# Performance work log

Hardware: AMD Instinct MI355X
Metric: run time of the kernel (lower is better)

Reference implementation:

```python
import jax, jax.numpy as jnp
import numpy as np

NUM_HEADS = 16
EMBED_DIM = 1024
HEAD_DIM = EMBED_DIM // NUM_HEADS
SCALE = HEAD_DIM * -0.5  # faithful to source: multiplicative, negative


def setup_inputs() -> dict:
    key = jax.random.key(0)
    kx, kq, kk, kv, ko = jax.random.split(key, 5)
    B, S, E = 2, 2048, EMBED_DIM
    std = 1.0 / np.sqrt(E)
    return {
        "x": jax.random.normal(kx, (B, S, E), dtype=jnp.float32),
        "Wq": jax.random.normal(kq, (E, E), dtype=jnp.float32) * std,
        "Wk": jax.random.normal(kk, (E, E), dtype=jnp.float32) * std,
        "Wv": jax.random.normal(kv, (E, E), dtype=jnp.float32) * std,
        "Wo": jax.random.normal(ko, (E, E), dtype=jnp.float32) * std,
    }


def reference(x, Wq, Wk, Wv, Wo):
    B, S, E = x.shape
    H, D = NUM_HEADS, HEAD_DIM
    # nn.Linear(bias=False): y = x @ W.T
    q = (x @ Wq.T).reshape(B, S, H, D).transpose(0, 2, 1, 3)  # unused downstream (faithful to source)
    k = (x @ Wk.T).reshape(B, S, H, D).transpose(0, 2, 1, 3)  # [B,H,S,D]
    v = (x @ Wv.T).reshape(B, S, H, D).transpose(0, 2, 1, 3)
    # Source bug reproduced: logits = K @ V^T, scaled by head_dim * -0.5
    logits = jnp.einsum('bhsd,bhtd->bhst', k, v) * SCALE  # [B,H,S,S]
    attn = jax.nn.softmax(logits, axis=-1)
    out = jnp.einsum('bhst,bhtd->bhsd', attn, v)  # [B,H,S,D]
    out = out.transpose(0, 2, 1, 3).reshape(B, S, E)
    return out @ Wo.T
```

## Files before the change

### kernel.cpp

```cpp
#include <hip/hip_runtime.h>
#include <math.h>

#define B_ 2
#define S_ 2048
#define E_ 1024
#define H_ 16
#define D_ 64
#define M_ (B_ * S_)
#define SC2 (-46.166241308446828f)

typedef unsigned short u16;
typedef __attribute__((ext_vector_type(8))) short short8;
typedef __attribute__((ext_vector_type(16))) float f32x16;

static __device__ __forceinline__ u16 bf16_rne(float x) {
    unsigned u = __float_as_uint(x);
    u += 0x7FFFu + ((u >> 16) & 1u);
    return (u16)(u >> 16);
}
static __device__ __forceinline__ float bf16f(u16 h) {
    return __uint_as_float(((unsigned)h) << 16);
}
static __device__ __forceinline__ f32x16 mfma_b(short8 a, short8 b, f32x16 c) {
    return __builtin_amdgcn_mfma_f32_32x32x16_bf16(a, b, c, 0, 0, 0);
}
static __device__ __forceinline__ unsigned pack2(u16 a, u16 b) {
    return (unsigned)a | ((unsigned)b << 16);
}
static __device__ __forceinline__ unsigned pack_trunc(float a, float b) {
    return __builtin_amdgcn_perm(__float_as_uint(b), __float_as_uint(a), 0x07060302u);
}
#define ROWMAP(r, hh) (((r) & 3) + ((((r) >> 2)) << 3) + ((hh) << 2))

__global__ __launch_bounds__(256)
void convert_split(const float* __restrict__ x, const float* __restrict__ Wk,
                   const float* __restrict__ Wv, const float* __restrict__ Wo,
                   u16* __restrict__ Xh, u16* __restrict__ Xl,
                   u16* __restrict__ Wkh, u16* __restrict__ Wkl,
                   u16* __restrict__ Wvh, u16* __restrict__ Wvl,
                   u16* __restrict__ Woh, u16* __restrict__ Wol)
{
    const int blk = blockIdx.x;
    const float* src; u16 *dh, *dl; int base; float sc = 1.0f;
    if (blk < 4096)      { src = x;  dh = Xh;  dl = Xl;  base = blk; }
    else if (blk < 5120) { src = Wk; dh = Wkh; dl = Wkl; base = blk - 4096; sc = SC2; }
    else if (blk < 6144) { src = Wv; dh = Wvh; dl = Wvl; base = blk - 5120; }
    else                 { src = Wo; dh = Woh; dl = Wol; base = blk - 6144; }
    const size_t off = ((size_t)base * 256 + threadIdx.x) * 4;
    const float4 v = *(const float4*)(src + off);
    const float f[4] = {v.x * sc, v.y * sc, v.z * sc, v.w * sc};
    u16 h4[4], l4[4];
#pragma unroll
    for (int i = 0; i < 4; ++i) {
        h4[i] = bf16_rne(f[i]);
        l4[i] = bf16_rne(f[i] - bf16f(h4[i]));
    }
    *(uint2*)(dh + off) = make_uint2(pack2(h4[0], h4[1]), pack2(h4[2], h4[3]));
    *(uint2*)(dl + off) = make_uint2(pack2(l4[0], l4[1]), pack2(l4[2], l4[3]));
}

#define CSB 1032
#define ARR (4 * CSB)

template<int MODE>
__global__ __launch_bounds__(512, 2)
void gemm_k(const u16* __restrict__ Ah, const u16* __restrict__ Al,
            const u16* __restrict__ B1h, const u16* __restrict__ B1l,
            const u16* __restrict__ B2h, const u16* __restrict__ B2l,
            u16* __restrict__ Khg, u16* __restrict__ Klg,
            u16* __restrict__ Vhg, u16* __restrict__ Vlg,
            u16* __restrict__ Vtg, float* __restrict__ Cout)
{
    __shared__ u16 stage[(MODE == 0 ? 6 : 4) * ARR];

    const int tid = threadIdx.x;
    const int w = tid >> 6, l31 = tid & 31, hh = (tid >> 5) & 1;
    const int wt = w & 3, ws = w >> 2;
    const int wm = (wt >> 1) << 6, wn = (wt & 1) << 6;
    const int m0 = blockIdx.y * 128, n0 = blockIdx.x * 128;
    const int ch = (ws << 1) + hh;

    const int srow = tid >> 2;
    const int sch  = tid & 3;
    const size_t gA = (size_t)(m0 + srow) * E_ + (sch << 3);
    const size_t gB = (size_t)(n0 + srow) * E_ + (sch << 3);
    const int slo = sch * CSB + srow * 8;

    f32x16 acc1[2][2], acc2[2][2];
#pragma unroll
    for (int mt = 0; mt < 2; ++mt)
#pragma unroll
        for (int nt = 0; nt < 2; ++nt)
#pragma unroll
            for (int r = 0; r < 16; ++r) {
                acc1[mt][nt][r] = 0.f;
                if constexpr (MODE == 0) acc2[mt][nt][r] = 0.f;
            }

    short8 pf[6];
    auto load_tile = [&](int k0) {
        pf[0] = *(const short8*)(Ah + gA + k0);
        pf[2] = *(const short8*)(B1h + gB + k0);
        if constexpr (MODE == 0) {
            pf[1] = *(const short8*)(Al + gA + k0);
            pf[3] = *(const short8*)(B1l + gB + k0);
            pf[4] = *(const short8*)(B2h + gB + k0);
            pf[5] = *(const short8*)(B2l + gB + k0);
        }
    };
    auto store_tile = [&]() {
        *(short8*)&stage[0 * ARR + slo] = pf[0];
        *(short8*)&stage[2 * ARR + slo] = pf[2];
        if constexpr (MODE == 0) {
            *(short8*)&stage[1 * ARR + slo] = pf[1];
            *(short8*)&stage[3 * ARR + slo] = pf[3];
            *(short8*)&stage[4 * ARR + slo] = pf[4];
            *(short8*)&stage[5 * ARR + slo] = pf[5];
        }
    };

    load_tile(0);
    for (int it = 0; it < 32; ++it) {
        store_tile();
        __syncthreads();
        if (it + 1 < 32) load_tile((it + 1) << 5);

        const int aoff = ch * CSB;
        short8 a_h[2], a_l[2];
        a_h[0] = *(const short8*)&stage[0 * ARR + aoff + (wm + l31) * 8];
        a_h[1] = *(const short8*)&stage[0 * ARR + aoff + (wm + 32 + l31) * 8];
        if constexpr (MODE == 0) {
            a_l[0] = *(const short8*)&stage[1 * ARR + aoff + (wm + l31) * 8];
            a_l[1] = *(const short8*)&stage[1 * ARR + aoff + (wm + 32 + l31) * 8];
        }
#pragma unroll
        for (int nt = 0; nt < 2; ++nt) {
            const int ro = aoff + (wn + (nt << 5) + l31) * 8;
            const short8 b1h = *(const short8*)&stage[2 * ARR + ro];
            if constexpr (MODE == 0) {
                const short8 b1l = *(const short8*)&stage[3 * ARR + ro];
                const short8 b2h = *(const short8*)&stage[4 * ARR + ro];
                const short8 b2l = *(const short8*)&stage[5 * ARR + ro];
#pragma unroll
                for (int mt = 0; mt < 2; ++mt) {
                    acc1[mt][nt] = mfma_b(a_h[mt], b1h, acc1[mt][nt]);
                    acc1[mt][nt] = mfma_b(a_h[mt], b1l, acc1[mt][nt]);
                    acc1[mt][nt] = mfma_b(a_l[mt], b1h, acc1[mt][nt]);
                    acc2[mt][nt] = mfma_b(a_h[mt], b2h, acc2[mt][nt]);
                    acc2[mt][nt] = mfma_b(a_h[mt], b2l, acc2[mt][nt]);
                    acc2[mt][nt] = mfma_b(a_l[mt], b2h, acc2[mt][nt]);
                }
            } else {
#pragma unroll
                for (int mt = 0; mt < 2; ++mt)
                    acc1[mt][nt] = mfma_b(a_h[mt], b1h, acc1[mt][nt]);
            }
        }
        __syncthreads();
    }

    float* red = (float*)stage;
    auto merge = [&](f32x16 (&acc)[2][2]) {
#pragma unroll
        for (int mt = 0; mt < 2; ++mt) {
            __syncthreads();
            if (ws == 1) {
#pragma unroll
                for (int nt = 0; nt < 2; ++nt)
#pragma unroll
                    for (int r = 0; r < 16; ++r)
                        red[wt * 2048 + ROWMAP(r, hh) * 64 + (nt << 5) + l31] = acc[mt][nt][r];
            }
            __syncthreads();
            if (ws == 0) {
#pragma unroll
                for (int nt = 0; nt < 2; ++nt)
#pragma unroll
                    for (int r = 0; r < 16; ++r)
                        acc[mt][nt][r] += red[wt * 2048 + ROWMAP(r, hh) * 64 + (nt << 5) + l31];
            }
        }
    };
    merge(acc1);
    if constexpr (MODE == 0) merge(acc2);

    if (ws != 0) return;

#pragma unroll
    for (int nt = 0; nt < 2; ++nt) {
        const int n = n0 + wn + (nt << 5) + l31;
        if constexpr (MODE == 1) {
#pragma unroll
            for (int mt = 0; mt < 2; ++mt)
#pragma unroll
                for (int r = 0; r < 16; ++r) {
                    const int m = m0 + wm + (mt << 5) + ROWMAP(r, hh);
                    Cout[(size_t)m * E_ + n] = acc1[mt][nt][r];
                }
        } else {
            const int hd = n >> 6, d = n & 63;
            const int b = m0 >> 11;
#pragma unroll
            for (int mt = 0; mt < 2; ++mt) {
                u16 vhi[16];
#pragma unroll
                for (int r = 0; r < 16; ++r) {
                    const int s = (m0 + wm + (mt << 5) + ROWMAP(r, hh)) & (S_ - 1);
                    const size_t ib = (((size_t)(b * H_ + hd) << 11) + s) * D_ + d;
                    const float kv = acc1[mt][nt][r];
                    const u16 kh_ = bf16_rne(kv);
                    Khg[ib] = kh_;
                    Klg[ib] = bf16_rne(kv - bf16f(kh_));
                    const float vv = acc2[mt][nt][r];
                    const u16 vh_ = bf16_rne(vv);
                    vhi[r] = vh_;
                    Vhg[ib] = vh_;
                    Vlg[ib] = bf16_rne(vv - bf16f(vh_));
                }
                const size_t vtb = ((size_t)(b * H_ + hd) * D_ + d) << 11;
#pragma unroll
                for (int g = 0; g < 4; ++g) {
                    const int s0 = ((m0 + wm + (mt << 5)) & (S_ - 1)) + (g << 3) + (hh << 2);
                    *(uint2*)&Vtg[vtb + s0] =
                        make_uint2(pack2(vhi[4 * g], vhi[4 * g + 1]),
                                   pack2(vhi[4 * g + 2], vhi[4 * g + 3]));
                }
            }
        }
    }
}

#define CSA 520
#define VA  (8 * CSA)
#define CSP 264
#define PW  (8 * CSP)

__global__ __launch_bounds__(512, 2)
void attn_mfma(const u16* __restrict__ Kh, const u16* __restrict__ Kl,
               const u16* __restrict__ Vh, const u16* __restrict__ Vl,
               const u16* __restrict__ Vt, u16* __restrict__ Obuf)
{
    __shared__ u16 sV[3 * VA];
    __shared__ u16 sP[8][PW];
    __shared__ float Alpha[8][32], Linv[8][32];

    const int tid = threadIdx.x;
    const int w = tid >> 6, l31 = tid & 31, hh = (tid >> 5) & 1;
    const int bh = blockIdx.y;
    const int sbase = blockIdx.x * 256 + (w << 5);
    const int sg = sbase + l31;

    short8 kfh[4], kfl[4];
    {
        const size_t kb = ((size_t)bh * S_ + sg) * D_;
#pragma unroll
        for (int ks = 0; ks < 4; ++ks) {
            const int db = (ks << 4) + (hh << 3);
            kfh[ks] = *(const short8*)(Kh + kb + db);
            kfl[ks] = *(const short8*)(Kl + kb + db);
        }
    }

    f32x16 oacc[2];
#pragma unroll
    for (int r = 0; r < 16; ++r) { oacc[0][r] = 0.f; oacc[1][r] = 0.f; }
    float m_i = -INFINITY, l_i = 0.f;

    const int rr = tid >> 3, cc = tid & 7;
    const size_t gn = ((size_t)bh * S_ + rr) * D_ + (cc << 3);
    const size_t gt = ((size_t)bh * D_ + rr) * S_ + (cc << 3);
    const int slo = cc * CSA + rr * 8;
    u16* P = &sP[w][0];

    short8 pv[3];
    auto load_tile = [&](int t0) {
        pv[0] = *(const short8*)(Vh + gn + (size_t)t0 * D_);
        pv[1] = *(const short8*)(Vl + gn + (size_t)t0 * D_);
        pv[2] = *(const short8*)(Vt + gt + t0);
    };

    load_tile(0);
    for (int it = 0; it < 32; ++it) {
        *(short8*)&sV[slo] = pv[0];
        *(short8*)&sV[VA + slo] = pv[1];
        *(short8*)&sV[2 * VA + slo] = pv[2];
        __syncthreads();
        if (it + 1 < 32) load_tile((it + 1) << 6);

        f32x16 st[2];
#pragma unroll
        for (int r = 0; r < 16; ++r) { st[0][r] = 0.f; st[1][r] = 0.f; }
#pragma unroll
        for (int ks = 0; ks < 4; ++ks) {
            const int ch = (ks << 1) + hh;
#pragma unroll
            for (int mt = 0; mt < 2; ++mt) {
                const int ro = ch * CSA + ((mt << 5) + l31) * 8;
                const short8 avh = *(const short8*)&sV[ro];
                const short8 avl = *(const short8*)&sV[VA + ro];
                st[mt] = mfma_b(avh, kfh[ks], st[mt]);
                st[mt] = mfma_b(avh, kfl[ks], st[mt]);
                st[mt] = mfma_b(avl, kfh[ks], st[mt]);
            }
        }

        float tmax = -INFINITY;
#pragma unroll
        for (int mt = 0; mt < 2; ++mt)
#pragma unroll
            for (int r = 0; r < 16; ++r) tmax = fmaxf(tmax, st[mt][r]);
        tmax = fmaxf(tmax, __shfl_xor(tmax, 32));
        const float mnew = fmaxf(m_i, tmax);
        const float alpha = __builtin_amdgcn_exp2f(m_i - mnew);
        m_i = mnew;
        const unsigned long long cmask = __ballot(tmax >= mnew - 30.f);

        if (cmask) {
            float rsum = 0.f;
#pragma unroll
            for (int mt = 0; mt < 2; ++mt)
#pragma unroll
                for (int r = 0; r < 16; ++r) {
                    const float p = __builtin_amdgcn_exp2f(st[mt][r] - mnew);
                    st[mt][r] = p;
                    rsum += p;
                }
            rsum += __shfl_xor(rsum, 32);
            l_i = l_i * alpha + rsum;
        }
        if (__ballot(alpha != 1.0f)) {
            if (hh == 0) Alpha[w][l31] = alpha;
#pragma unroll
            for (int g = 0; g < 4; ++g) {
                const float4 av = *(const float4*)&Alpha[w][(g << 3) + (hh << 2)];
                const float af[4] = {av.x, av.y, av.z, av.w};
#pragma unroll
                for (int q = 0; q < 4; ++q) {
                    oacc[0][(g << 2) + q] *= af[q];
                    oacc[1][(g << 2) + q] *= af[q];
                }
            }
        }
        if (cmask) {
#pragma unroll
            for (int mt = 0; mt < 2; ++mt)
#pragma unroll
                for (int g = 0; g < 4; ++g)
                    *(uint2*)&P[((mt << 2) + g) * CSP + l31 * 8 + (hh << 2)] =
                        make_uint2(pack_trunc(st[mt][4 * g], st[mt][4 * g + 1]),
                                   pack_trunc(st[mt][4 * g + 2], st[mt][4 * g + 3]));
#pragma unroll
            for (int ks = 0; ks < 4; ++ks) {
                const int ch = (ks << 1) + hh;
                const short8 pfr = *(const short8*)&P[ch * CSP + l31 * 8];
#pragma unroll
                for (int nt = 0; nt < 2; ++nt) {
                    const short8 vtf = *(const short8*)&sV[2 * VA + ch * CSA + ((nt << 5) + l31) * 8];
                    oacc[nt] = mfma_b(pfr, vtf, oacc[nt]);
                }
            }
        }
        __syncthreads();
    }

    if (hh == 0) Linv[w][l31] = 1.0f / l_i;
    const int b = bh >> 4;
    const int hd = bh & 15;
    u16* Or = Obuf + ((size_t)b * S_ + sbase) * E_ + (hd << 6);
#pragma unroll
    for (int g = 0; g < 4; ++g) {
        const float4 iv = *(const float4*)&Linv[w][(g << 3) + (hh << 2)];
        const float invs[4] = {iv.x, iv.y, iv.z, iv.w};
#pragma unroll
        for (int nt = 0; nt < 2; ++nt)
#pragma unroll
            for (int q = 0; q < 4; ++q) {
                const int sl = (g << 3) + (hh << 2) + q;
                Or[(size_t)sl * E_ + (nt << 5) + l31] =
                    bf16_rne(oacc[nt][(g << 2) + q] * invs[q]);
            }
    }
}

extern "C" void kernel_launch(void* const* d_in, const int* in_sizes, int n_in,
                              void* d_out, int out_size, void* d_ws, size_t ws_size,
                              hipStream_t stream)
{
    (void)in_sizes; (void)n_in; (void)out_size; (void)ws_size;
    const float* x  = (const float*)d_in[0];
    const float* Wk = (const float*)d_in[2];
    const float* Wv = (const float*)d_in[3];
    const float* Wo = (const float*)d_in[4];
    float* out = (float*)d_out;

    char* ws = (char*)d_ws;
    const size_t MB = 1u << 20;
    u16* Xh  = (u16*)(ws + 0 * MB);
    u16* Xl  = (u16*)(ws + 8 * MB);
    u16* Wkh = (u16*)(ws + 16 * MB);
    u16* Wkl = (u16*)(ws + 18 * MB);
    u16* Wvh = (u16*)(ws + 20 * MB);
    u16* Wvl = (u16*)(ws + 22 * MB);
    u16* Woh = (u16*)(ws + 24 * MB);
    u16* Kh  = (u16*)(ws + 26 * MB);
    u16* Kl  = (u16*)(ws + 34 * MB);
    u16* Vh  = (u16*)(ws + 42 * MB);
    u16* Vl  = (u16*)(ws + 50 * MB);
    u16* Vt  = (u16*)(ws + 58 * MB);
    u16* Obuf = Xl;
    u16* Wol_junk = Kh;

    convert_split<<<7168, 256, 0, stream>>>(x, Wk, Wv, Wo,
                                            Xh, Xl, Wkh, Wkl, Wvh, Wvl, Woh, Wol_junk);
    gemm_k<0><<<dim3(E_ / 128, M_ / 128), 512, 0, stream>>>(
        Xh, Xl, Wkh, Wkl, Wvh, Wvl, Kh, Kl, Vh, Vl, Vt, nullptr);
    attn_mfma<<<dim3(S_ / 256, B_ * H_), 512, 0, stream>>>(Kh, Kl, Vh, Vl, Vt, Obuf);
    gemm_k<1><<<dim3(E_ / 128, M_ / 128), 512, 0, stream>>>(
        Obuf, Obuf, Woh, Woh, Woh, Woh,
        nullptr, nullptr, nullptr, nullptr, nullptr, out);
}
```

Measured before the change: 226.9 us.

## Switch split-precision pipeline from bf16 to fp16 and drop V low part

Replaces the bf16 hi/lo split with an fp16 hi/lo split throughout the projections and attention. The extra mantissa bits of fp16 let the attention logits drop the V-low correction term, going from three MFMAs to two per step, and remove the Vl buffer and its LDS stage. The projection GEMMs also move to 256-thread blocks where each wave covers a 128x64 tile. This cuts MFMA work, memory traffic and LDS usage, at the cost of fp16 range risk and fewer waves per block.

```diff
diff --git a/kernel.cpp b/kernel.cpp
--- a/kernel.cpp
+++ b/kernel.cpp
@@ -10,25 +10,23 @@
 #define SC2 (-46.166241308446828f)
 
 typedef unsigned short u16;
-typedef __attribute__((ext_vector_type(8))) short short8;
+typedef _Float16 f16;
+typedef __attribute__((ext_vector_type(8))) _Float16 f16x8;
+typedef __attribute__((ext_vector_type(2))) __fp16 fp16x2_n;
 typedef __attribute__((ext_vector_type(16))) float f32x16;
 
-static __device__ __forceinline__ u16 bf16_rne(float x) {
-    unsigned u = __float_as_uint(x);
-    u += 0x7FFFu + ((u >> 16) & 1u);
-    return (u16)(u >> 16);
-}
-static __device__ __forceinline__ float bf16f(u16 h) {
-    return __uint_as_float(((unsigned)h) << 16);
-}
-static __device__ __forceinline__ f32x16 mfma_b(short8 a, short8 b, f32x16 c) {
-    return __builtin_amdgcn_mfma_f32_32x32x16_bf16(a, b, c, 0, 0, 0);
+static __device__ __forceinline__ f32x16 mfma_h(f16x8 a, f16x8 b, f32x16 c) {
+    return __builtin_amdgcn_mfma_f32_32x32x16_f16(a, b, c, 0, 0, 0);
+}
+static __device__ __forceinline__ u16 f16bits(f16 h) {
+    union { f16 h; u16 u; } c; c.h = h; return c.u;
 }
 static __device__ __forceinline__ unsigned pack2(u16 a, u16 b) {
     return (unsigned)a | ((unsigned)b << 16);
 }
-static __device__ __forceinline__ unsigned pack_trunc(float a, float b) {
-    return __builtin_amdgcn_perm(__float_as_uint(b), __float_as_uint(a), 0x07060302u);
+static __device__ __forceinline__ unsigned pkrtz(float a, float b) {
+    fp16x2_n h = __builtin_amdgcn_cvt_pkrtz(a, b);
+    unsigned u; __builtin_memcpy(&u, &h, 4); return u;
 }
 #define ROWMAP(r, hh) (((r) & 3) + ((((r) >> 2)) << 3) + ((hh) << 2))
 
@@ -52,8 +50,9 @@
     u16 h4[4], l4[4];
 #pragma unroll
     for (int i = 0; i < 4; ++i) {
-        h4[i] = bf16_rne(f[i]);
-        l4[i] = bf16_rne(f[i] - bf16f(h4[i]));
+        const f16 h = (f16)f[i];
+        h4[i] = f16bits(h);
+        l4[i] = f16bits((f16)(f[i] - (float)h));
     }
     *(uint2*)(dh + off) = make_uint2(pack2(h4[0], h4[1]), pack2(h4[2], h4[3]));
     *(uint2*)(dl + off) = make_uint2(pack2(l4[0], l4[1]), pack2(l4[2], l4[3]));
@@ -63,32 +62,33 @@
 #define ARR (4 * CSB)
 
 template<int MODE>
-__global__ __launch_bounds__(512, 2)
-void gemm_k(const u16* __restrict__ Ah, const u16* __restrict__ Al,
-            const u16* __restrict__ B1h, const u16* __restrict__ B1l,
-            const u16* __restrict__ B2h, const u16* __restrict__ B2l,
+__global__ __launch_bounds__(256, 1)
+void gemm_f(const u16* __restrict__ Ah_, const u16* __restrict__ Al_,
+            const u16* __restrict__ B1h_, const u16* __restrict__ B1l_,
+            const u16* __restrict__ B2h_, const u16* __restrict__ B2l_,
             u16* __restrict__ Khg, u16* __restrict__ Klg,
-            u16* __restrict__ Vhg, u16* __restrict__ Vlg,
-            u16* __restrict__ Vtg, float* __restrict__ Cout)
+            u16* __restrict__ Vhg, u16* __restrict__ Vtg,
+            float* __restrict__ Cout)
 {
-    __shared__ u16 stage[(MODE == 0 ? 6 : 4) * ARR];
+    constexpr int NARR = (MODE == 0 ? 6 : 2);
+    __shared__ u16 stage[NARR * ARR];
 
     const int tid = threadIdx.x;
     const int w = tid >> 6, l31 = tid & 31, hh = (tid >> 5) & 1;
-    const int wt = w & 3, ws = w >> 2;
-    const int wm = (wt >> 1) << 6, wn = (wt & 1) << 6;
+    const int ws = w >> 1;
+    const int wn = (w & 1) << 6;
     const int m0 = blockIdx.y * 128, n0 = blockIdx.x * 128;
-    const int ch = (ws << 1) + hh;
-
-    const int srow = tid >> 2;
-    const int sch  = tid & 3;
-    const size_t gA = (size_t)(m0 + srow) * E_ + (sch << 3);
-    const size_t gB = (size_t)(n0 + srow) * E_ + (sch << 3);
-    const int slo = sch * CSB + srow * 8;
-
-    f32x16 acc1[2][2], acc2[2][2];
-#pragma unroll
-    for (int mt = 0; mt < 2; ++mt)
+    const int ch8 = (ws << 1) + hh;
+
+    const int sr = tid >> 1, c0 = (tid & 1) << 1;
+    const size_t gA = (size_t)(m0 + sr) * E_ + (c0 << 3);
+    const size_t gB = (size_t)(n0 + sr) * E_ + (c0 << 3);
+    const int lo0 = c0 * CSB + sr * 8;
+    const int lo1 = (c0 + 1) * CSB + sr * 8;
+
+    f32x16 acc1[4][2], acc2[4][2];
+#pragma unroll
+    for (int mt = 0; mt < 4; ++mt)
 #pragma unroll
         for (int nt = 0; nt < 2; ++nt)
 #pragma unroll
@@ -97,25 +97,25 @@
                 if constexpr (MODE == 0) acc2[mt][nt][r] = 0.f;
             }
 
-    short8 pf[6];
+    f16x8 pf[2 * NARR];
+    const u16* gptr[6];
+    gptr[0] = Ah_; gptr[1] = Al_; gptr[2] = B1h_;
+    gptr[3] = B1l_; gptr[4] = B2h_; gptr[5] = B2l_;
+
     auto load_tile = [&](int k0) {
-        pf[0] = *(const short8*)(Ah + gA + k0);
-        pf[2] = *(const short8*)(B1h + gB + k0);
-        if constexpr (MODE == 0) {
-            pf[1] = *(const short8*)(Al + gA + k0);
-            pf[3] = *(const short8*)(B1l + gB + k0);
-            pf[4] = *(const short8*)(B2h + gB + k0);
-            pf[5] = *(const short8*)(B2l + gB + k0);
+#pragma unroll
+        for (int a = 0; a < NARR; ++a) {
+            const size_t g = ((MODE == 0 && a < 2) || (MODE == 1 && a < 1)) ? gA : gB;
+            const u16* p = (MODE == 1 && a == 1) ? B1h_ : gptr[a];
+            pf[2 * a + 0] = *(const f16x8*)(p + g + k0);
+            pf[2 * a + 1] = *(const f16x8*)(p + g + k0 + 8);
         }
     };
     auto store_tile = [&]() {
-        *(short8*)&stage[0 * ARR + slo] = pf[0];
-        *(short8*)&stage[2 * ARR + slo] = pf[2];
-        if constexpr (MODE == 0) {
-            *(short8*)&stage[1 * ARR + slo] = pf[1];
-            *(short8*)&stage[3 * ARR + slo] = pf[3];
-            *(short8*)&stage[4 * ARR + slo] = pf[4];
-            *(short8*)&stage[5 * ARR + slo] = pf[5];
+#pragma unroll
+        for (int a = 0; a < NARR; ++a) {
+            *(f16x8*)&stage[a * ARR + lo0] = pf[2 * a + 0];
+            *(f16x8*)&stage[a * ARR + lo1] = pf[2 * a + 1];
         }
     };
 
@@ -125,65 +125,67 @@
         __syncthreads();
         if (it + 1 < 32) load_tile((it + 1) << 5);
 
-        const int aoff = ch * CSB;
-        short8 a_h[2], a_l[2];
-        a_h[0] = *(const short8*)&stage[0 * ARR + aoff + (wm + l31) * 8];
-        a_h[1] = *(const short8*)&stage[0 * ARR + aoff + (wm + 32 + l31) * 8];
-        if constexpr (MODE == 0) {
-            a_l[0] = *(const short8*)&stage[1 * ARR + aoff + (wm + l31) * 8];
-            a_l[1] = *(const short8*)&stage[1 * ARR + aoff + (wm + 32 + l31) * 8];
+        f16x8 xh[4], xl[4];
+#pragma unroll
+        for (int mt = 0; mt < 4; ++mt) {
+            const int off = ch8 * CSB + ((mt << 5) + l31) * 8;
+            xh[mt] = *(const f16x8*)&stage[0 * ARR + off];
+            if constexpr (MODE == 0)
+                xl[mt] = *(const f16x8*)&stage[1 * ARR + off];
         }
 #pragma unroll
         for (int nt = 0; nt < 2; ++nt) {
-            const int ro = aoff + (wn + (nt << 5) + l31) * 8;
-            const short8 b1h = *(const short8*)&stage[2 * ARR + ro];
+            const int boff = ch8 * CSB + (wn + (nt << 5) + l31) * 8;
             if constexpr (MODE == 0) {
-                const short8 b1l = *(const short8*)&stage[3 * ARR + ro];
-                const short8 b2h = *(const short8*)&stage[4 * ARR + ro];
-                const short8 b2l = *(const short8*)&stage[5 * ARR + ro];
-#pragma unroll
-                for (int mt = 0; mt < 2; ++mt) {
-                    acc1[mt][nt] = mfma_b(a_h[mt], b1h, acc1[mt][nt]);
-                    acc1[mt][nt] = mfma_b(a_h[mt], b1l, acc1[mt][nt]);
-                    acc1[mt][nt] = mfma_b(a_l[mt], b1h, acc1[mt][nt]);
-                    acc2[mt][nt] = mfma_b(a_h[mt], b2h, acc2[mt][nt]);
-                    acc2[mt][nt] = mfma_b(a_h[mt], b2l, acc2[mt][nt]);
-                    acc2[mt][nt] = mfma_b(a_l[mt], b2h, acc2[mt][nt]);
+                const f16x8 b1h = *(const f16x8*)&stage[2 * ARR + boff];
+                const f16x8 b1l = *(const f16x8*)&stage[3 * ARR + boff];
+                const f16x8 b2h = *(const f16x8*)&stage[4 * ARR + boff];
+                const f16x8 b2l = *(const f16x8*)&stage[5 * ARR + boff];
+#pragma unroll
+                for (int mt = 0; mt < 4; ++mt) {
+                    acc1[mt][nt] = mfma_h(xh[mt], b1h, acc1[mt][nt]);
+                    acc1[mt][nt] = mfma_h(xh[mt], b1l, acc1[mt][nt]);
+                    acc1[mt][nt] = mfma_h(xl[mt], b1h, acc1[mt][nt]);
+                    acc2[mt][nt] = mfma_h(xh[mt], b2h, acc2[mt][nt]);
+                    acc2[mt][nt] = mfma_h(xh[mt], b2l, acc2[mt][nt]);
+                    acc2[mt][nt] = mfma_h(xl[mt], b2h, acc2[mt][nt]);
                 }
             } else {
-#pragma unroll
-                for (int mt = 0; mt < 2; ++mt)
-                    acc1[mt][nt] = mfma_b(a_h[mt], b1h, acc1[mt][nt]);
+                const f16x8 b1h = *(const f16x8*)&stage[1 * ARR + boff];
+#pragma unroll
+                for (int mt = 0; mt < 4; ++mt)
+                    acc1[mt][nt] = mfma_h(xh[mt], b1h, acc1[mt][nt]);
             }
         }
         __syncthreads();
     }
 
     float* red = (float*)stage;
-    auto merge = [&](f32x16 (&acc)[2][2]) {
-#pragma unroll
-        for (int mt = 0; mt < 2; ++mt) {
+#pragma unroll
+    for (int ai = 0; ai < (MODE == 0 ? 2 : 1); ++ai) {
+#pragma unroll
+        for (int mt = 0; mt < 4; ++mt) {
             __syncthreads();
             if (ws == 1) {
 #pragma unroll
                 for (int nt = 0; nt < 2; ++nt)
 #pragma unroll
                     for (int r = 0; r < 16; ++r)
-                        red[wt * 2048 + ROWMAP(r, hh) * 64 + (nt << 5) + l31] = acc[mt][nt][r];
+                        red[ROWMAP(r, hh) * 128 + wn + (nt << 5) + l31] =
+                            (ai == 0) ? acc1[mt][nt][r] : acc2[mt][nt][r];
             }
             __syncthreads();
             if (ws == 0) {
 #pragma unroll
                 for (int nt = 0; nt < 2; ++nt)
 #pragma unroll
-                    for (int r = 0; r < 16; ++r)
-                        acc[mt][nt][r] += red[wt * 2048 + ROWMAP(r, hh) * 64 + (nt << 5) + l31];
-            }
-        }
-    };
-    merge(acc1);
-    if constexpr (MODE == 0) merge(acc2);
-
+                    for (int r = 0; r < 16; ++r) {
+                        const float p = red[ROWMAP(r, hh) * 128 + wn + (nt << 5) + l31];
+                        if (ai == 0) acc1[mt][nt][r] += p; else acc2[mt][nt][r] += p;
+                    }
+            }
+        }
+    }
     if (ws != 0) return;
 
 #pragma unroll
@@ -191,39 +193,37 @@
         const int n = n0 + wn + (nt << 5) + l31;
         if constexpr (MODE == 1) {
 #pragma unroll
-            for (int mt = 0; mt < 2; ++mt)
+            for (int mt = 0; mt < 4; ++mt)
 #pragma unroll
                 for (int r = 0; r < 16; ++r) {
-                    const int m = m0 + wm + (mt << 5) + ROWMAP(r, hh);
+                    const int m = m0 + (mt << 5) + ROWMAP(r, hh);
                     Cout[(size_t)m * E_ + n] = acc1[mt][nt][r];
                 }
         } else {
             const int hd = n >> 6, d = n & 63;
             const int b = m0 >> 11;
 #pragma unroll
-            for (int mt = 0; mt < 2; ++mt) {
-                u16 vhi[16];
+            for (int mt = 0; mt < 4; ++mt) {
+                u16 vb[16];
 #pragma unroll
                 for (int r = 0; r < 16; ++r) {
-                    const int s = (m0 + wm + (mt << 5) + ROWMAP(r, hh)) & (S_ - 1);
+                    const int s = (m0 + (mt << 5) + ROWMAP(r, hh)) & (S_ - 1);
                     const size_t ib = (((size_t)(b * H_ + hd) << 11) + s) * D_ + d;
                     const float kv = acc1[mt][nt][r];
-                    const u16 kh_ = bf16_rne(kv);
-                    Khg[ib] = kh_;
-                    Klg[ib] = bf16_rne(kv - bf16f(kh_));
-                    const float vv = acc2[mt][nt][r];
-                    const u16 vh_ = bf16_rne(vv);
-                    vhi[r] = vh_;
-                    Vhg[ib] = vh_;
-                    Vlg[ib] = bf16_rne(vv - bf16f(vh_));
+                    const f16 kh = (f16)kv;
+                    Khg[ib] = f16bits(kh);
+                    Klg[ib] = f16bits((f16)(kv - (float)kh));
+                    const f16 vh = (f16)acc2[mt][nt][r];
+                    vb[r] = f16bits(vh);
+                    Vhg[ib] = vb[r];
                 }
                 const size_t vtb = ((size_t)(b * H_ + hd) * D_ + d) << 11;
 #pragma unroll
                 for (int g = 0; g < 4; ++g) {
-                    const int s0 = ((m0 + wm + (mt << 5)) & (S_ - 1)) + (g << 3) + (hh << 2);
+                    const int s0 = ((m0 + (mt << 5)) & (S_ - 1)) + (g << 3) + (hh << 2);
                     *(uint2*)&Vtg[vtb + s0] =
-                        make_uint2(pack2(vhi[4 * g], vhi[4 * g + 1]),
-                                   pack2(vhi[4 * g + 2], vhi[4 * g + 3]));
+                        make_uint2(pack2(vb[4 * g], vb[4 * g + 1]),
+                                   pack2(vb[4 * g + 2], vb[4 * g + 3]));
                 }
             }
         }
@@ -237,10 +237,10 @@
 
 __global__ __launch_bounds__(512, 2)
 void attn_mfma(const u16* __restrict__ Kh, const u16* __restrict__ Kl,
-               const u16* __restrict__ Vh, const u16* __restrict__ Vl,
-               const u16* __restrict__ Vt, u16* __restrict__ Obuf)
+               const u16* __restrict__ Vh, const u16* __restrict__ Vt,
+               u16* __restrict__ Obuf)
 {
-    __shared__ u16 sV[3 * VA];
+    __shared__ u16 sV[2 * VA];
     __shared__ u16 sP[8][PW];
     __shared__ float Alpha[8][32], Linv[8][32];
 
@@ -250,14 +250,14 @@
     const int sbase = blockIdx.x * 256 + (w << 5);
     const int sg = sbase + l31;
 
-    short8 kfh[4], kfl[4];
+    f16x8 kfh[4], kfl[4];
     {
         const size_t kb = ((size_t)bh * S_ + sg) * D_;
 #pragma unroll
         for (int ks = 0; ks < 4; ++ks) {
             const int db = (ks << 4) + (hh << 3);
-            kfh[ks] = *(const short8*)(Kh + kb + db);
-            kfl[ks] = *(const short8*)(Kl + kb + db);
+            kfh[ks] = *(const f16x8*)(Kh + kb + db);
+            kfl[ks] = *(const f16x8*)(Kl + kb + db);
         }
     }
 
@@ -272,18 +272,16 @@
     const int slo = cc * CSA + rr * 8;
     u16* P = &sP[w][0];
 
-    short8 pv[3];
+    f16x8 pv[2];
     auto load_tile = [&](int t0) {
-        pv[0] = *(const short8*)(Vh + gn + (size_t)t0 * D_);
-        pv[1] = *(const short8*)(Vl + gn + (size_t)t0 * D_);
-        pv[2] = *(const short8*)(Vt + gt + t0);
+        pv[0] = *(const f16x8*)(Vh + gn + (size_t)t0 * D_);
+        pv[1] = *(const f16x8*)(Vt + gt + t0);
     };
 
     load_tile(0);
     for (int it = 0; it < 32; ++it) {
-        *(short8*)&sV[slo] = pv[0];
-        *(short8*)&sV[VA + slo] = pv[1];
-        *(short8*)&sV[2 * VA + slo] = pv[2];
+        *(f16x8*)&sV[slo] = pv[0];
+        *(f16x8*)&sV[VA + slo] = pv[1];
         __syncthreads();
         if (it + 1 < 32) load_tile((it + 1) << 6);
 
@@ -295,12 +293,9 @@
             const int ch = (ks << 1) + hh;
 #pragma unroll
             for (int mt = 0; mt < 2; ++mt) {
-                const int ro = ch * CSA + ((mt << 5) + l31) * 8;
-                const short8 avh = *(const short8*)&sV[ro];
-                const short8 avl = *(const short8*)&sV[VA + ro];
-                st[mt] = mfma_b(avh, kfh[ks], st[mt]);
-                st[mt] = mfma_b(avh, kfl[ks], st[mt]);
-                st[mt] = mfma_b(avl, kfh[ks], st[mt]);
+                const f16x8 av = *(const f16x8*)&sV[ch * CSA + ((mt << 5) + l31) * 8];
+                st[mt] = mfma_h(av, kfh[ks], st[mt]);
+                st[mt] = mfma_h(av, kfl[ks], st[mt]);
             }
         }
 
@@ -347,16 +342,16 @@
 #pragma unroll
                 for (int g = 0; g < 4; ++g)
                     *(uint2*)&P[((mt << 2) + g) * CSP + l31 * 8 + (hh << 2)] =
-                        make_uint2(pack_trunc(st[mt][4 * g], st[mt][4 * g + 1]),
-                                   pack_trunc(st[mt][4 * g + 2], st[mt][4 * g + 3]));
+                        make_uint2(pkrtz(st[mt][4 * g], st[mt][4 * g + 1]),
+                                   pkrtz(st[mt][4 * g + 2], st[mt][4 * g + 3]));
 #pragma unroll
             for (int ks = 0; ks < 4; ++ks) {
                 const int ch = (ks << 1) + hh;
-                const short8 pfr = *(const short8*)&P[ch * CSP + l31 * 8];
+                const f16x8 pfr = *(const f16x8*)&P[ch * CSP + l31 * 8];
 #pragma unroll
                 for (int nt = 0; nt < 2; ++nt) {
-                    const short8 vtf = *(const short8*)&sV[2 * VA + ch * CSA + ((nt << 5) + l31) * 8];
-                    oacc[nt] = mfma_b(pfr, vtf, oacc[nt]);
+                    const f16x8 vtf = *(const f16x8*)&sV[VA + ch * CSA + ((nt << 5) + l31) * 8];
+                    oacc[nt] = mfma_h(pfr, vtf, oacc[nt]);
                 }
             }
         }
@@ -377,7 +372,7 @@
             for (int q = 0; q < 4; ++q) {
                 const int sl = (g << 3) + (hh << 2) + q;
                 Or[(size_t)sl * E_ + (nt << 5) + l31] =
-                    bf16_rne(oacc[nt][(g << 2) + q] * invs[q]);
+                    f16bits((f16)(oacc[nt][(g << 2) + q] * invs[q]));
             }
     }
 }
@@ -403,19 +398,18 @@
     u16* Wvl = (u16*)(ws + 22 * MB);
     u16* Woh = (u16*)(ws + 24 * MB);
     u16* Kh  = (u16*)(ws + 26 * MB);
-    u16* Kl  = (u16*)(ws + 34 * MB);
-    u16* Vh  = (u16*)(ws + 42 * MB);
-    u16* Vl  = (u16*)(ws + 50 * MB);
-    u16* Vt  = (u16*)(ws + 58 * MB);
+    u16* Kl  = (u16*)(ws + 35 * MB);
+    u16* Vh  = (u16*)(ws + 44 * MB);
+    u16* Vt  = (u16*)(ws + 53 * MB);
     u16* Obuf = Xl;
     u16* Wol_junk = Kh;
 
     convert_split<<<7168, 256, 0, stream>>>(x, Wk, Wv, Wo,
                                             Xh, Xl, Wkh, Wkl, Wvh, Wvl, Woh, Wol_junk);
-    gemm_k<0><<<dim3(E_ / 128, M_ / 128), 512, 0, stream>>>(
-        Xh, Xl, Wkh, Wkl, Wvh, Wvl, Kh, Kl, Vh, Vl, Vt, nullptr);
-    attn_mfma<<<dim3(S_ / 256, B_ * H_), 512, 0, stream>>>(Kh, Kl, Vh, Vl, Vt, Obuf);
-    gemm_k<1><<<dim3(E_ / 128, M_ / 128), 512, 0, stream>>>(
+    gemm_f<0><<<dim3(E_ / 128, M_ / 128), 256, 0, stream>>>(
+        Xh, Xl, Wkh, Wkl, Wvh, Wvl, Kh, Kl, Vh, Vt, nullptr);
+    attn_mfma<<<dim3(S_ / 256, B_ * H_), 512, 0, stream>>>(Kh, Kl, Vh, Vt, Obuf);
+    gemm_f<1><<<dim3(E_ / 128, M_ / 128), 256, 0, stream>>>(
         Obuf, Obuf, Woh, Woh, Woh, Woh,
-        nullptr, nullptr, nullptr, nullptr, nullptr, out);
-}
+        nullptr, nullptr, nullptr, nullptr, out);
+}
```

Result: slower. 239.2 us (+5.4%).
